# Kernel tuning notes

Hardware: AMD Instinct MI355X
Metric: run time of the kernel (lower is better)

The kernel has to match this reference:

```python
import jax, jax.numpy as jnp
import numpy as np
import math

EMBED_DIM = 1024
NUM_HEADS = 4
HEAD_DIM = EMBED_DIM // NUM_HEADS
B, N = 4, 2048


def setup_inputs() -> dict:
    key = jax.random.key(0)
    ks = jax.random.split(key, 5)
    s = 1.0 / math.sqrt(EMBED_DIM)
    return {
        "x": jax.random.normal(ks[0], (B, N, EMBED_DIM), dtype=jnp.float32),
        "w_qkv": jax.random.normal(ks[1], (EMBED_DIM, 3 * EMBED_DIM), dtype=jnp.float32) * s,
        "b_qkv": jnp.zeros((3 * EMBED_DIM,), dtype=jnp.float32),
        "w_out": jax.random.normal(ks[2], (EMBED_DIM, EMBED_DIM), dtype=jnp.float32) * s,
        "b_out": jnp.zeros((EMBED_DIM,), dtype=jnp.float32),
        "ln_gamma": jnp.ones((EMBED_DIM,), dtype=jnp.float32),
        "ln_beta": jnp.zeros((EMBED_DIM,), dtype=jnp.float32),
    }


def reference(x, w_qkv, b_qkv, w_out, b_out, ln_gamma, ln_beta):
    Bx, Nx, D = x.shape
    qkv = x @ w_qkv + b_qkv  # [B, N, 3D]
    q, k, v = jnp.split(qkv, 3, axis=-1)
    # [B, H, N, hd]
    def heads(t):
        return t.reshape(Bx, Nx, NUM_HEADS, HEAD_DIM).transpose(0, 2, 1, 3)
    q, k, v = heads(q), heads(k), heads(v)
    scale = 1.0 / math.sqrt(HEAD_DIM)
    attn = jnp.einsum("bhqd,bhkd->bhqk", q, k) * scale  # [B, H, N, N]
    attn = jax.nn.softmax(attn, axis=-1)
    out = jnp.einsum("bhqk,bhkd->bhqd", attn, v)  # [B, H, N, hd]
    out = out.transpose(0, 2, 1, 3).reshape(Bx, Nx, D)
    out = out @ w_out + b_out
    # residual + LayerNorm (eps=1e-5 like torch default)
    y = x + out
    mu = jnp.mean(y, axis=-1, keepdims=True)
    var = jnp.mean(jnp.square(y - mu), axis=-1, keepdims=True)
    y = (y - mu) * jax.lax.rsqrt(var + 1e-5)
    return y * ln_gamma + ln_beta
```

## Files before the change

kernel.cpp:

```cpp
#include <hip/hip_runtime.h>
#include <hip/hip_bf16.h>

typedef __attribute__((ext_vector_type(8))) short short8;
typedef __attribute__((ext_vector_type(4))) float f32x4;
typedef __attribute__((ext_vector_type(16))) float f32x16;
typedef __attribute__((ext_vector_type(4))) unsigned uint4v;

#define GLOB_AS __attribute__((address_space(1)))
#define LDS_AS  __attribute__((address_space(3)))

__device__ __forceinline__ void async16(void* lds, const void* g) {
  __builtin_amdgcn_global_load_lds((const GLOB_AS unsigned int*)g,
                                   (LDS_AS unsigned int*)lds, 16, 0, 0);
}

__device__ __forceinline__ unsigned short f2bf(float f) {
  unsigned u = __float_as_uint(f);
  unsigned r = u + 0x7FFFu + ((u >> 16) & 1u);
  return (unsigned short)(r >> 16);
}

__device__ __forceinline__ float bf2f(unsigned short u) {
  unsigned x = ((unsigned)u) << 16;
  return __uint_as_float(x);
}

__device__ __forceinline__ unsigned pk2(float lo, float hi) {
  __hip_bfloat162 h = __float22bfloat162_rn(float2{lo, hi});
  return *reinterpret_cast<unsigned*>(&h);
}

__device__ __forceinline__ void lane32_swap(unsigned& a, unsigned& b, int lane) {
#if __has_builtin(__builtin_amdgcn_permlane32_swap)
  auto r = __builtin_amdgcn_permlane32_swap(a, b, false, false);
  a = r[0]; b = r[1];
#else
  unsigned tb = __shfl_xor(b, 32);
  unsigned ta = __shfl_xor(a, 32);
  unsigned na = (lane < 32) ? a : tb;
  unsigned nb = (lane < 32) ? ta : b;
  a = na; b = nb;
#endif
}

#define BATCH 4
#define SEQ   2048
#define DMODEL 1024
#define NHEAD 4
#define HD    256

#define QSCALE 0.090169944f
#define FIXM 24.0f

__global__ __launch_bounds__(256) void cast_bf16_kernel(
    const float* __restrict__ in, unsigned short* __restrict__ out) {
  int i = blockIdx.x * 256 + threadIdx.x;
  float4 v = ((const float4*)in)[i];
  uint2 o;
  o.x = (unsigned)f2bf(v.x) | ((unsigned)f2bf(v.y) << 16);
  o.y = (unsigned)f2bf(v.z) | ((unsigned)f2bf(v.w) << 16);
  ((uint2*)out)[i] = o;
}

__global__ __launch_bounds__(256) void transpose_cast_kernel(
    const float* __restrict__ in, unsigned short* __restrict__ out, int R, int C) {
  __shared__ float tile[32][33];
  int c0 = blockIdx.x * 32, r0 = blockIdx.y * 32;
  int tx = threadIdx.x, ty = threadIdx.y;
#pragma unroll
  for (int i = 0; i < 4; ++i)
    tile[ty + 8 * i][tx] = in[(size_t)(r0 + ty + 8 * i) * C + c0 + tx];
  __syncthreads();
#pragma unroll
  for (int i = 0; i < 4; ++i)
    out[(size_t)(c0 + ty + 8 * i) * R + r0 + tx] = f2bf(tile[tx][ty + 8 * i]);
}

__global__ __launch_bounds__(256) void gemm_qkv_kernel(
    const unsigned short* __restrict__ A,
    const unsigned short* __restrict__ Bt,
    const float* __restrict__ bias,
    unsigned short* __restrict__ qb,
    unsigned short* __restrict__ kb,
    unsigned short* __restrict__ vt) {
  __shared__ __align__(16) unsigned short sA[2][128 * 32];
  __shared__ __align__(16) unsigned short sB[2][128 * 32];
  const int t = threadIdx.x;
  const int l = t & 63, w = t >> 6;
  const int g = l >> 4, lr = l & 15;
  const int wr = w >> 1, wc = w & 1;
  const int bid = blockIdx.x;
  const int xcd = bid & 7, sub = bid >> 3;
  const int bxl = sub % 3, by = sub / 3;
  const int row0 = by * 128;
  const int col0 = (xcd * 3 + bxl) * 128;

  auto stage = [&](int buf, int kt) {
#pragma unroll
    for (int i = 0; i < 2; ++i) {
      int e = i * 256 + t;
      async16(&sA[buf][e * 8], A + (size_t)(row0 + (e >> 2)) * 1024 + kt + (e & 3) * 8);
      async16(&sB[buf][e * 8], Bt + (size_t)(col0 + (e >> 2)) * 1024 + kt + (e & 3) * 8);
    }
  };

  stage(0, 0);

  f32x4 acc[4][4] = {};
  for (int ki = 0; ki < 32; ++ki) {
    const int cur = ki & 1;
    __syncthreads();
    if (ki < 31) stage(cur ^ 1, (ki + 1) * 32);
    short8 af[4], bf[4];
#pragma unroll
    for (int m = 0; m < 4; ++m)
      af[m] = *(const short8*)&sA[cur][(wr * 64 + m * 16 + lr) * 32 + g * 8];
#pragma unroll
    for (int n = 0; n < 4; ++n)
      bf[n] = *(const short8*)&sB[cur][(wc * 64 + n * 16 + lr) * 32 + g * 8];
    __builtin_amdgcn_s_setprio(1);
#pragma unroll
    for (int m = 0; m < 4; ++m)
#pragma unroll
      for (int n = 0; n < 4; ++n)
        acc[m][n] = __builtin_amdgcn_mfma_f32_16x16x32_bf16(af[m], bf[n], acc[m][n], 0, 0, 0);
    __builtin_amdgcn_s_setprio(0);
  }

#pragma unroll
  for (int m = 0; m < 4; ++m) {
    int rowb = row0 + wr * 64 + m * 16 + g * 4;
    int b = rowb >> 11;
    int nb = rowb & 2047;
#pragma unroll
    for (int nn = 0; nn < 4; ++nn) {
      int col = col0 + wc * 64 + nn * 16 + lr;
      float bv = bias[col];
      int sec = col >> 10, c1 = col & 1023;
      int h = c1 >> 8, d = c1 & 255;
      if (sec == 2) {
        unsigned short p0 = f2bf(acc[m][nn][0] + bv);
        unsigned short p1 = f2bf(acc[m][nn][1] + bv);
        unsigned short p2 = f2bf(acc[m][nn][2] + bv);
        unsigned short p3 = f2bf(acc[m][nn][3] + bv);
        uint2 pk;
        pk.x = (unsigned)p0 | ((unsigned)p1 << 16);
        pk.y = (unsigned)p2 | ((unsigned)p3 << 16);
        size_t idx = (((size_t)((b * NHEAD + h) * 128 + (nb >> 4))) * 256 + d) * 16 + (nb & 15);
        *(uint2*)&vt[idx] = pk;
      } else {
        unsigned short* dst = (sec == 0) ? qb : kb;
        float sc = (sec == 0) ? QSCALE : 1.0f;
#pragma unroll
        for (int rr = 0; rr < 4; ++rr) {
          size_t idx = ((size_t)((b * NHEAD + h) * SEQ + nb + rr)) * HD + d;
          dst[idx] = f2bf((acc[m][nn][rr] + bv) * sc);
        }
      }
    }
  }
}

__global__ __launch_bounds__(256, 2) void attn_kernel(
    const unsigned short* __restrict__ qb,
    const unsigned short* __restrict__ kb,
    const unsigned short* __restrict__ vt,
    unsigned short* __restrict__ Oh,
    float* __restrict__ st) {
  __shared__ __align__(16) unsigned short sK[2][32 * 256];
  __shared__ __align__(16) unsigned short sV[2][2 * 256 * 16];
  const int t = threadIdx.x, l = t & 63, w = t >> 6;
  const int row = l & 31, hi = l >> 5;
  const int swz = row << 4;
  const int bid = blockIdx.x;
  const int bh = (bid & 7) * 2 + ((bid >> 3) & 1);
  const int qblk = (bid >> 4) & 15;
  const int kvhalf = bid >> 8;
  const int b = bh >> 2, h = bh & 3;
  const int q = qblk * 128 + w * 32 + row;
  const unsigned short* Qp = qb + (size_t)bh * SEQ * HD;
  const char* Kg = (const char*)(kb + (size_t)bh * SEQ * HD);
  const char* Vg = (const char*)(vt + (size_t)bh * (128 * 256 * 16));

  short8 qf[16];
#pragma unroll
  for (int dc = 0; dc < 16; ++dc)
    qf[dc] = *(const short8*)&Qp[(size_t)q * HD + dc * 16 + hi * 8];

  auto stage = [&](int buf, int kp0) {
#pragma unroll
    for (int i = 0; i < 4; ++i) {
      int s = i * 256 + t;
      int r = s >> 5;
      int colb = (s & 31) * 16;
      int src = (kp0 + r) * 512 + (colb ^ (r << 4));
      async16((char*)sK[buf] + s * 16, Kg + src);
    }
    const int c0 = kp0 >> 4;
#pragma unroll
    for (int i = 0; i < 4; ++i) {
      int s = i * 256 + t;
      int kh = s >> 9, rem = s & 511;
      int d = rem >> 1, vhi = rem & 1;
      int src = ((c0 + kh) * 256 + d) * 32 + vhi * 16;
      async16((char*)sV[buf] + s * 16, Vg + src);
    }
  };

  stage(0, kvhalf * 32);
  __syncthreads();

  f32x16 O[8] = {};
  float lsum = 0.f;

  for (int it = 0; it < 32; ++it) {
    const int kp0 = (2 * it + kvhalf) * 32;
    const int cur = it & 1;
    if (it < 31) stage(cur ^ 1, kp0 + 64);

    f32x16 Sa = {}, Sb = {};
    const char* sKc = (const char*)sK[cur];
    __builtin_amdgcn_s_setprio(1);
#pragma unroll
    for (int dc = 0; dc < 16; dc += 2) {
      short8 kf0 = *(const short8*)(sKc + row * 512 + ((dc * 32 + hi * 16) ^ swz));
      short8 kf1 = *(const short8*)(sKc + row * 512 + (((dc + 1) * 32 + hi * 16) ^ swz));
      Sa = __builtin_amdgcn_mfma_f32_32x32x16_bf16(kf0, qf[dc], Sa, 0, 0, 0);
      Sb = __builtin_amdgcn_mfma_f32_32x32x16_bf16(kf1, qf[dc + 1], Sb, 0, 0, 0);
    }
    __builtin_amdgcn_s_setprio(0);

    float e[16];
#pragma unroll
    for (int i = 0; i < 16; ++i) e[i] = exp2f((Sa[i] + Sb[i]) - FIXM);
    float s0 = (e[0] + e[1]) + (e[2] + e[3]);
    float s1 = (e[4] + e[5]) + (e[6] + e[7]);
    float s2 = (e[8] + e[9]) + (e[10] + e[11]);
    float s3 = (e[12] + e[13]) + (e[14] + e[15]);
    lsum += (s0 + s1) + (s2 + s3);

    unsigned a0 = pk2(e[0], e[1]),   a1 = pk2(e[2], e[3]);
    unsigned b0 = pk2(e[4], e[5]),   b1 = pk2(e[6], e[7]);
    unsigned c0 = pk2(e[8], e[9]),   c1 = pk2(e[10], e[11]);
    unsigned d0 = pk2(e[12], e[13]), d1 = pk2(e[14], e[15]);
    lane32_swap(a0, b0, l);
    lane32_swap(a1, b1, l);
    lane32_swap(c0, d0, l);
    lane32_swap(c1, d1, l);
    uint4v u1; u1.x = a0; u1.y = a1; u1.z = b0; u1.w = b1;
    uint4v u2; u2.x = c0; u2.y = c1; u2.z = d0; u2.w = d1;
    short8 pf1 = __builtin_bit_cast(short8, u1);
    short8 pf2 = __builtin_bit_cast(short8, u2);

    const char* sVc = (const char*)sV[cur];
    __builtin_amdgcn_s_setprio(1);
#pragma unroll
    for (int db = 0; db < 8; ++db) {
      short8 vf0 = *(const short8*)(sVc + ((db * 32 + row) * 2 + hi) * 16);
      O[db] = __builtin_amdgcn_mfma_f32_32x32x16_bf16(vf0, pf1, O[db], 0, 0, 0);
    }
#pragma unroll
    for (int db = 0; db < 8; ++db) {
      short8 vf1 = *(const short8*)(sVc + 8192 + ((db * 32 + row) * 2 + hi) * 16);
      O[db] = __builtin_amdgcn_mfma_f32_32x32x16_bf16(vf1, pf2, O[db], 0, 0, 0);
    }
    __builtin_amdgcn_s_setprio(0);

    __syncthreads();
  }

  lsum += __shfl_xor(lsum, 32);
  float inv = 1.0f / lsum;
  unsigned short* aop = Oh + (size_t)kvhalf * (8192ull * 1024);
  size_t obase = ((size_t)(b * SEQ + q)) * DMODEL + h * HD;
#pragma unroll
  for (int db = 0; db < 8; ++db)
#pragma unroll
    for (int rg = 0; rg < 4; ++rg) {
      int dd = db * 32 + rg * 8 + hi * 4;
      uint2 pk;
      pk.x = pk2(O[db][rg * 4 + 0] * inv, O[db][rg * 4 + 1] * inv);
      pk.y = pk2(O[db][rg * 4 + 2] * inv, O[db][rg * 4 + 3] * inv);
      *(uint2*)&aop[obase + dd] = pk;
    }
  if (hi == 0)
    st[((size_t)kvhalf * 16 + bh) * 2048 + q] = lsum;
}

__global__ __launch_bounds__(256) void combine_kernel(
    const unsigned short* __restrict__ Oh,
    const float* __restrict__ st,
    unsigned short* __restrict__ ao) {
  int rowg = blockIdx.x, t = threadIdx.x;
  int b = rowg >> 11, q = rowg & 2047;
  int col = t * 4;
  int bh = b * 4 + (col >> 8);
  float l0 = st[(size_t)bh * 2048 + q];
  float l1 = st[(16ull * 2048) + (size_t)bh * 2048 + q];
  float inv = 1.0f / (l0 + l1);
  float w0 = l0 * inv, w1 = l1 * inv;
  size_t base = (size_t)rowg * 1024 + col;
  uint2 ua = *(const uint2*)&Oh[base];
  uint2 ub = *(const uint2*)&Oh[8192ull * 1024 + base];
  unsigned short oa[4] = {(unsigned short)(ua.x & 0xFFFF), (unsigned short)(ua.x >> 16),
                          (unsigned short)(ua.y & 0xFFFF), (unsigned short)(ua.y >> 16)};
  unsigned short ob[4] = {(unsigned short)(ub.x & 0xFFFF), (unsigned short)(ub.x >> 16),
                          (unsigned short)(ub.y & 0xFFFF), (unsigned short)(ub.y >> 16)};
  float r[4];
#pragma unroll
  for (int j = 0; j < 4; ++j) r[j] = w0 * bf2f(oa[j]) + w1 * bf2f(ob[j]);
  uint2 pk;
  pk.x = pk2(r[0], r[1]);
  pk.y = pk2(r[2], r[3]);
  *(uint2*)&ao[base] = pk;
}

__global__ __launch_bounds__(256) void gemm_out_kernel(
    const unsigned short* __restrict__ A,
    const unsigned short* __restrict__ Bt,
    const float* __restrict__ bias,
    const float* __restrict__ x,
    unsigned short* __restrict__ y) {
  __shared__ __align__(16) unsigned short sA[2][128 * 32];
  __shared__ __align__(16) unsigned short sB[2][128 * 32];
  const int t = threadIdx.x;
  const int l = t & 63, w = t >> 6;
  const int g = l >> 4, lr = l & 15;
  const int wr = w >> 1, wc = w & 1;
  const int bid = blockIdx.x;
  const int xcd = bid & 7, by = bid >> 3;
  const int row0 = by * 128;
  const int col0 = xcd * 128;

  auto stage = [&](int buf, int kt) {
#pragma unroll
    for (int i = 0; i < 2; ++i) {
      int e = i * 256 + t;
      async16(&sA[buf][e * 8], A + (size_t)(row0 + (e >> 2)) * 1024 + kt + (e & 3) * 8);
      async16(&sB[buf][e * 8], Bt + (size_t)(col0 + (e >> 2)) * 1024 + kt + (e & 3) * 8);
    }
  };

  stage(0, 0);

  f32x4 acc[4][4] = {};
  for (int ki = 0; ki < 32; ++ki) {
    const int cur = ki & 1;
    __syncthreads();
    if (ki < 31) stage(cur ^ 1, (ki + 1) * 32);
    short8 af[4], bf[4];
#pragma unroll
    for (int m = 0; m < 4; ++m)
      af[m] = *(const short8*)&sA[cur][(wr * 64 + m * 16 + lr) * 32 + g * 8];
#pragma unroll
    for (int n = 0; n < 4; ++n)
      bf[n] = *(const short8*)&sB[cur][(wc * 64 + n * 16 + lr) * 32 + g * 8];
    __builtin_amdgcn_s_setprio(1);
#pragma unroll
    for (int m = 0; m < 4; ++m)
#pragma unroll
      for (int n = 0; n < 4; ++n)
        acc[m][n] = __builtin_amdgcn_mfma_f32_16x16x32_bf16(af[m], bf[n], acc[m][n], 0, 0, 0);
    __builtin_amdgcn_s_setprio(0);
  }

#pragma unroll
  for (int m = 0; m < 4; ++m) {
    int rowb = row0 + wr * 64 + m * 16 + g * 4;
#pragma unroll
    for (int nn = 0; nn < 4; ++nn) {
      int col = col0 + wc * 64 + nn * 16 + lr;
      float bv = bias[col];
#pragma unroll
      for (int rr = 0; rr < 4; ++rr) {
        size_t idx = (size_t)(rowb + rr) * 1024 + col;
        y[idx] = f2bf(acc[m][nn][rr] + bv + x[idx]);
      }
    }
  }
}

__global__ __launch_bounds__(256) void ln_kernel(
    const unsigned short* __restrict__ y, const float* __restrict__ gamma,
    const float* __restrict__ beta, float* __restrict__ out) {
  int row = blockIdx.x, t = threadIdx.x;
  uint2 u = ((const uint2*)(y + (size_t)row * 1024))[t];
  float v0 = bf2f((unsigned short)(u.x & 0xFFFF));
  float v1 = bf2f((unsigned short)(u.x >> 16));
  float v2 = bf2f((unsigned short)(u.y & 0xFFFF));
  float v3 = bf2f((unsigned short)(u.y >> 16));
  float s = v0 + v1 + v2 + v3;
  float qs = v0 * v0 + v1 * v1 + v2 * v2 + v3 * v3;
#pragma unroll
  for (int off = 1; off < 64; off <<= 1) {
    s += __shfl_xor(s, off);
    qs += __shfl_xor(qs, off);
  }
  __shared__ float ss[4], qq[4];
  if ((t & 63) == 0) { ss[t >> 6] = s; qq[t >> 6] = qs; }
  __syncthreads();
  s = ss[0] + ss[1] + ss[2] + ss[3];
  qs = qq[0] + qq[1] + qq[2] + qq[3];
  float mean = s * (1.0f / 1024.0f);
  float var = qs * (1.0f / 1024.0f) - mean * mean;
  float rstd = rsqrtf(var + 1e-5f);
  float4 gm = ((const float4*)gamma)[t];
  float4 bt = ((const float4*)beta)[t];
  float4 o;
  o.x = (v0 - mean) * rstd * gm.x + bt.x;
  o.y = (v1 - mean) * rstd * gm.y + bt.y;
  o.z = (v2 - mean) * rstd * gm.z + bt.z;
  o.w = (v3 - mean) * rstd * gm.w + bt.w;
  ((float4*)(out + (size_t)row * 1024))[t] = o;
}

extern "C" void kernel_launch(void* const* d_in, const int* in_sizes, int n_in,
                              void* d_out, int out_size, void* d_ws, size_t ws_size,
                              hipStream_t stream) {
  const float* x      = (const float*)d_in[0];
  const float* w_qkv  = (const float*)d_in[1];
  const float* b_qkv  = (const float*)d_in[2];
  const float* w_out  = (const float*)d_in[3];
  const float* b_out  = (const float*)d_in[4];
  const float* gamma  = (const float*)d_in[5];
  const float* beta   = (const float*)d_in[6];
  float* out = (float*)d_out;

  char* ws = (char*)d_ws;
  unsigned short* xb    = (unsigned short*)(ws);
  unsigned short* wqkvT = (unsigned short*)(ws + (16u << 20));
  unsigned short* woutT = (unsigned short*)(ws + (22u << 20));
  unsigned short* qb    = (unsigned short*)(ws + (24u << 20));
  unsigned short* kb    = (unsigned short*)(ws + (40u << 20));
  unsigned short* vt    = (unsigned short*)(ws + (56u << 20));
  unsigned short* ao    = (unsigned short*)(ws + (72u << 20));
  unsigned short* Oh    = (unsigned short*)(ws + (88u << 20));
  unsigned short* y     = (unsigned short*)(ws + (88u << 20));
  float* st             = (float*)(ws + (16u << 20));

  cast_bf16_kernel<<<(BATCH * SEQ * DMODEL) / (256 * 4), 256, 0, stream>>>(x, xb);
  transpose_cast_kernel<<<dim3(96, 32), dim3(32, 8), 0, stream>>>(w_qkv, wqkvT, 1024, 3072);
  transpose_cast_kernel<<<dim3(32, 32), dim3(32, 8), 0, stream>>>(w_out, woutT, 1024, 1024);
  gemm_qkv_kernel<<<1536, 256, 0, stream>>>(xb, wqkvT, b_qkv, qb, kb, vt);
  attn_kernel<<<512, 256, 0, stream>>>(qb, kb, vt, Oh, st);
  combine_kernel<<<BATCH * SEQ, 256, 0, stream>>>(Oh, st, ao);
  gemm_out_kernel<<<512, 256, 0, stream>>>(ao, woutT, b_out, x, y);
  ln_kernel<<<BATCH * SEQ, 256, 0, stream>>>(y, gamma, beta, out);
}
```

Baseline: 245.2 us.

## Split attention KV range into three partitions with single-buffered V staging

The attention kernel now splits the key/value sequence three ways instead of two, launching 768 blocks rather than 512 and raising the occupancy hint to three blocks per CU. V is single-buffered and staged inside each iteration behind an extra barrier, which shrinks LDS so three blocks fit per CU. The combine kernel merges three partial outputs, and the workspace layout is rearranged to hold the third partial buffer. The goal is more parallel blocks to fill the GPU, at the cost of V load latency no longer being hidden, an extra sync per iteration, and more combine traffic.

```diff
diff --git a/kernel.cpp b/kernel.cpp
--- a/kernel.cpp
+++ b/kernel.cpp
@@ -161,21 +161,22 @@
   }
 }
 
-__global__ __launch_bounds__(256, 2) void attn_kernel(
+__global__ __launch_bounds__(256, 3) void attn_kernel(
     const unsigned short* __restrict__ qb,
     const unsigned short* __restrict__ kb,
     const unsigned short* __restrict__ vt,
     unsigned short* __restrict__ Oh,
     float* __restrict__ st) {
   __shared__ __align__(16) unsigned short sK[2][32 * 256];
-  __shared__ __align__(16) unsigned short sV[2][2 * 256 * 16];
+  __shared__ __align__(16) unsigned short sV[2 * 256 * 16];
   const int t = threadIdx.x, l = t & 63, w = t >> 6;
   const int row = l & 31, hi = l >> 5;
   const int swz = row << 4;
   const int bid = blockIdx.x;
   const int bh = (bid & 7) * 2 + ((bid >> 3) & 1);
-  const int qblk = (bid >> 4) & 15;
-  const int kvhalf = bid >> 8;
+  const int rest = bid >> 4;
+  const int qblk = rest & 15;
+  const int third = rest >> 4;
   const int b = bh >> 2, h = bh & 3;
   const int q = qblk * 128 + w * 32 + row;
   const unsigned short* Qp = qb + (size_t)bh * SEQ * HD;
@@ -187,7 +188,7 @@
   for (int dc = 0; dc < 16; ++dc)
     qf[dc] = *(const short8*)&Qp[(size_t)q * HD + dc * 16 + hi * 8];
 
-  auto stage = [&](int buf, int kp0) {
+  auto stageK = [&](int buf, int kp0) {
 #pragma unroll
     for (int i = 0; i < 4; ++i) {
       int s = i * 256 + t;
@@ -196,6 +197,8 @@
       int src = (kp0 + r) * 512 + (colb ^ (r << 4));
       async16((char*)sK[buf] + s * 16, Kg + src);
     }
+  };
+  auto stageV = [&](int kp0) {
     const int c0 = kp0 >> 4;
 #pragma unroll
     for (int i = 0; i < 4; ++i) {
@@ -203,20 +206,22 @@
       int kh = s >> 9, rem = s & 511;
       int d = rem >> 1, vhi = rem & 1;
       int src = ((c0 + kh) * 256 + d) * 32 + vhi * 16;
-      async16((char*)sV[buf] + s * 16, Vg + src);
+      async16((char*)sV + s * 16, Vg + src);
     }
   };
 
-  stage(0, kvhalf * 32);
+  stageK(0, third * 32);
   __syncthreads();
 
   f32x16 O[8] = {};
   float lsum = 0.f;
 
-  for (int it = 0; it < 32; ++it) {
-    const int kp0 = (2 * it + kvhalf) * 32;
-    const int cur = it & 1;
-    if (it < 31) stage(cur ^ 1, kp0 + 64);
+  int i = 0;
+  for (int c = third; c < 64; c += 3, ++i) {
+    const int kp0 = c * 32;
+    const int cur = i & 1;
+    stageV(kp0);
+    if (c + 3 < 64) stageK(cur ^ 1, (c + 3) * 32);
 
     f32x16 Sa = {}, Sb = {};
     const char* sKc = (const char*)sK[cur];
@@ -232,7 +237,7 @@
 
     float e[16];
 #pragma unroll
-    for (int i = 0; i < 16; ++i) e[i] = exp2f((Sa[i] + Sb[i]) - FIXM);
+    for (int ii = 0; ii < 16; ++ii) e[ii] = exp2f((Sa[ii] + Sb[ii]) - FIXM);
     float s0 = (e[0] + e[1]) + (e[2] + e[3]);
     float s1 = (e[4] + e[5]) + (e[6] + e[7]);
     float s2 = (e[8] + e[9]) + (e[10] + e[11]);
@@ -252,7 +257,9 @@
     short8 pf1 = __builtin_bit_cast(short8, u1);
     short8 pf2 = __builtin_bit_cast(short8, u2);
 
-    const char* sVc = (const char*)sV[cur];
+    __syncthreads();
+
+    const char* sVc = (const char*)sV;
     __builtin_amdgcn_s_setprio(1);
 #pragma unroll
     for (int db = 0; db < 8; ++db) {
@@ -271,7 +278,7 @@
 
   lsum += __shfl_xor(lsum, 32);
   float inv = 1.0f / lsum;
-  unsigned short* aop = Oh + (size_t)kvhalf * (8192ull * 1024);
+  unsigned short* aop = Oh + (size_t)third * (8192ull * 1024);
   size_t obase = ((size_t)(b * SEQ + q)) * DMODEL + h * HD;
 #pragma unroll
   for (int db = 0; db < 8; ++db)
@@ -284,7 +291,7 @@
       *(uint2*)&aop[obase + dd] = pk;
     }
   if (hi == 0)
-    st[((size_t)kvhalf * 16 + bh) * 2048 + q] = lsum;
+    st[((size_t)third * 16 + bh) * 2048 + q] = lsum;
 }
 
 __global__ __launch_bounds__(256) void combine_kernel(
@@ -297,18 +304,23 @@
   int bh = b * 4 + (col >> 8);
   float l0 = st[(size_t)bh * 2048 + q];
   float l1 = st[(16ull * 2048) + (size_t)bh * 2048 + q];
-  float inv = 1.0f / (l0 + l1);
-  float w0 = l0 * inv, w1 = l1 * inv;
+  float l2 = st[(32ull * 2048) + (size_t)bh * 2048 + q];
+  float inv = 1.0f / (l0 + l1 + l2);
+  float w0 = l0 * inv, w1 = l1 * inv, w2 = l2 * inv;
   size_t base = (size_t)rowg * 1024 + col;
   uint2 ua = *(const uint2*)&Oh[base];
   uint2 ub = *(const uint2*)&Oh[8192ull * 1024 + base];
+  uint2 uc = *(const uint2*)&Oh[2ull * 8192 * 1024 + base];
   unsigned short oa[4] = {(unsigned short)(ua.x & 0xFFFF), (unsigned short)(ua.x >> 16),
                           (unsigned short)(ua.y & 0xFFFF), (unsigned short)(ua.y >> 16)};
   unsigned short ob[4] = {(unsigned short)(ub.x & 0xFFFF), (unsigned short)(ub.x >> 16),
                           (unsigned short)(ub.y & 0xFFFF), (unsigned short)(ub.y >> 16)};
+  unsigned short oc[4] = {(unsigned short)(uc.x & 0xFFFF), (unsigned short)(uc.x >> 16),
+                          (unsigned short)(uc.y & 0xFFFF), (unsigned short)(uc.y >> 16)};
   float r[4];
 #pragma unroll
-  for (int j = 0; j < 4; ++j) r[j] = w0 * bf2f(oa[j]) + w1 * bf2f(ob[j]);
+  for (int j = 0; j < 4; ++j)
+    r[j] = w0 * bf2f(oa[j]) + w1 * bf2f(ob[j]) + w2 * bf2f(oc[j]);
   uint2 pk;
   pk.x = pk2(r[0], r[1]);
   pk.y = pk2(r[2], r[3]);
@@ -433,16 +445,16 @@
   unsigned short* qb    = (unsigned short*)(ws + (24u << 20));
   unsigned short* kb    = (unsigned short*)(ws + (40u << 20));
   unsigned short* vt    = (unsigned short*)(ws + (56u << 20));
-  unsigned short* ao    = (unsigned short*)(ws + (72u << 20));
-  unsigned short* Oh    = (unsigned short*)(ws + (88u << 20));
-  unsigned short* y     = (unsigned short*)(ws + (88u << 20));
+  unsigned short* Oh    = (unsigned short*)(ws + (72u << 20));
+  unsigned short* ao    = (unsigned short*)(ws);
+  unsigned short* y     = (unsigned short*)(ws + (72u << 20));
   float* st             = (float*)(ws + (16u << 20));
 
   cast_bf16_kernel<<<(BATCH * SEQ * DMODEL) / (256 * 4), 256, 0, stream>>>(x, xb);
   transpose_cast_kernel<<<dim3(96, 32), dim3(32, 8), 0, stream>>>(w_qkv, wqkvT, 1024, 3072);
   transpose_cast_kernel<<<dim3(32, 32), dim3(32, 8), 0, stream>>>(w_out, woutT, 1024, 1024);
   gemm_qkv_kernel<<<1536, 256, 0, stream>>>(xb, wqkvT, b_qkv, qb, kb, vt);
-  attn_kernel<<<512, 256, 0, stream>>>(qb, kb, vt, Oh, st);
+  attn_kernel<<<768, 256, 0, stream>>>(qb, kb, vt, Oh, st);
   combine_kernel<<<BATCH * SEQ, 256, 0, stream>>>(Oh, st, ao);
   gemm_out_kernel<<<512, 256, 0, stream>>>(ao, woutT, b_out, x, y);
   ln_kernel<<<BATCH * SEQ, 256, 0, stream>>>(y, gamma, beta, out);
```

New measurement: 480.1 us. 95.8% more time.
